# Performance work log

Hardware: AMD Instinct MI355X
Metric: run time of the kernel (lower is better)

## Reference

```python
import jax, jax.numpy as jnp
import numpy as np

N = 12288
E = 196608
H = 128
Z = 128
NEG = -1e9  # finite mask value (avoids -inf NaNs in grads)
WSCALE = 0.05


def setup_inputs() -> dict:
    key = jax.random.key(0)
    ks = jax.random.split(key, 16)
    inp = {}
    inp["x"] = jax.random.normal(ks[0], (N, 2), dtype=jnp.float32)
    inp["z"] = jax.random.normal(ks[1], (Z,), dtype=jnp.float32)
    inp["node_type"] = jax.random.randint(ks[2], (N,), 0, 3, dtype=jnp.int32)
    inp["node_depth"] = jax.random.randint(ks[3], (N,), 0, 64, dtype=jnp.int32)
    inp["edge_index"] = jax.random.randint(ks[4], (2, E), 0, N, dtype=jnp.int32)
    inp["W1"] = jax.random.normal(ks[5], (2, H), dtype=jnp.float32) * WSCALE
    inp["b1"] = jnp.zeros((H,), jnp.float32)
    inp["W2"] = jax.random.normal(ks[6], (H, H), dtype=jnp.float32) * WSCALE
    inp["b2"] = jnp.zeros((H,), jnp.float32)
    inp["Wm1"] = jax.random.normal(ks[7], (H + Z, H), dtype=jnp.float32) * WSCALE
    inp["bm1"] = jnp.zeros((H,), jnp.float32)
    inp["Wm2"] = jax.random.normal(ks[8], (H, H), dtype=jnp.float32) * WSCALE
    inp["bm2"] = jnp.zeros((H,), jnp.float32)
    inp["Ws"] = jax.random.normal(ks[9], (H, H), dtype=jnp.float32) * WSCALE
    inp["Wt"] = jax.random.normal(ks[10], (H, H), dtype=jnp.float32) * WSCALE
    inp["Wi1"] = jax.random.normal(ks[11], (2 * H + Z, H), dtype=jnp.float32) * WSCALE
    inp["bi1"] = jnp.zeros((H,), jnp.float32)
    inp["Wi2"] = jax.random.normal(ks[12], (H, 1), dtype=jnp.float32) * WSCALE
    inp["bi2"] = jnp.zeros((1,), jnp.float32)
    return inp


def _gcn(x, W, b, src, dst, n):
    # GCNConv with self-loops and symmetric deg^-1/2 normalization
    loop = jnp.arange(n, dtype=src.dtype)
    s = jnp.concatenate([src, loop])
    d = jnp.concatenate([dst, loop])
    deg = jax.ops.segment_sum(jnp.ones_like(d, dtype=x.dtype), d, num_segments=n)
    inv_sqrt = jnp.where(deg > 0, jax.lax.rsqrt(jnp.maximum(deg, 1.0)), 0.0)
    w = inv_sqrt[s] * inv_sqrt[d]  # [E+N]
    agg = jax.ops.segment_sum(x[s] * w[:, None], d, num_segments=n)  # [N,F]
    return agg @ W + b


def reference(x, z, node_type, node_depth, edge_index,
              W1, b1, W2, b2, Wm1, bm1, Wm2, bm2, Ws, Wt, Wi1, bi1, Wi2, bi2):
    n = x.shape[0]
    src, dst = edge_index[0], edge_index[1]
    # 2-layer GCN encode
    h = jax.nn.relu(_gcn(x, W1, b1, src, dst, n))
    h = jax.nn.relu(_gcn(h, W2, b2, src, dst, n))
    # node_mlp on [h, z] (no outer relu, per original edge_index branch)
    zb = jnp.broadcast_to(z, (n, Z))
    h = jax.nn.relu(jnp.concatenate([h, zb], axis=1) @ Wm1 + bm1) @ Wm2 + bm2  # [N,H]
    # batched score: St[v,u] = tgt_proj(h_v) . src_proj(h_u)
    St = (h @ Wt) @ (h @ Ws).T  # [N(target), N(candidate)]
    cand_ok = node_depth[None, :] < node_depth[:, None]  # candidate strictly shallower
    St = jnp.where(cand_ok, St, NEG)
    vals, idx = jax.lax.top_k(St, 2)  # [N,2] per-target top candidates
    # target is active if type != 0, depth > 0, and at least one candidate exists
    tv = (node_type != 0) & (node_depth > 0) & (vals[:, 0] > NEG / 2)
    # k=2 edges for AND nodes (type==2), else k=1
    edge_valid = jnp.stack([tv, tv & (node_type == 2)], axis=1)  # [N,2]
    # inversion bit mlp on [h_u, h_v, z]
    hu = h[idx]  # [N,2,H]
    hv = jnp.broadcast_to(h[:, None, :], hu.shape)
    zz = jnp.broadcast_to(z, (n, 2, Z))
    feat = jnp.concatenate([hu, hv, zz], axis=-1)  # [N,2,2H+Z]
    logit = (jax.nn.relu(feat @ Wi1 + bi1) @ Wi2 + bi2)[..., 0]  # [N,2]
    inv_prob = jax.nn.sigmoid(logit)
    return inv_prob, vals, idx, edge_valid
```

## Files before the change

### kernel.cpp

```cpp
#include <hip/hip_runtime.h>
#include <hip/hip_bf16.h>

#define NN 12288
#define NE 196608
#define HD 128
#define ZD 128
#define NEGV (-1.0e9f)
#define SEG 16

using s8v = __attribute__((ext_vector_type(8))) short;
using f4v = __attribute__((ext_vector_type(4))) float;
using i4v = __attribute__((ext_vector_type(4))) int;

__device__ __forceinline__ unsigned short f2bf(float f) {
    return __builtin_bit_cast(unsigned short, __float2bfloat16(f));
}
__device__ __forceinline__ float4 pack8(float4 a, float4 b) {
    unsigned p0 = ((unsigned)f2bf(a.y) << 16) | f2bf(a.x);
    unsigned p1 = ((unsigned)f2bf(a.w) << 16) | f2bf(a.z);
    unsigned p2 = ((unsigned)f2bf(b.y) << 16) | f2bf(b.x);
    unsigned p3 = ((unsigned)f2bf(b.w) << 16) | f2bf(b.z);
    i4v r = (i4v){(int)p0, (int)p1, (int)p2, (int)p3};
    return __builtin_bit_cast(float4, r);
}

__global__ __launch_bounds__(256) void k_counts_wz(
        const int* __restrict__ edst, const int* __restrict__ ndep,
        const float* __restrict__ W2, const float* __restrict__ Wm1,
        const float* __restrict__ Wm2, const float* __restrict__ Wtm,
        const float* __restrict__ Wsm, const float* __restrict__ Wi1,
        const float* __restrict__ z, const float* __restrict__ bm1,
        const float* __restrict__ bi1,
        int* degi, int* cnt, __hip_bfloat16* __restrict__ wt7,
        float* cz1, float* cz2) {
    __shared__ int lh[64];
    __shared__ float tl[16 * 129];
    int tid = threadIdx.x;
    int bid = blockIdx.x;
    if (bid < NE / 256) {
        int e = bid * 256 + tid;
        atomicAdd(&degi[edst[e]], 1);
    } else if (bid < NE / 256 + NN / 256) {
        if (tid < 64) lh[tid] = 0;
        __syncthreads();
        int v = (bid - NE / 256) * 256 + tid;
        atomicAdd(&lh[ndep[v]], 1);
        __syncthreads();
        if (tid < 64) {
            int c = lh[tid];
            if (c) atomicAdd(&cnt[tid * 16], c);
        }
    } else if (bid < NE / 256 + NN / 256 + 56) {
        int b2 = bid - NE / 256 - NN / 256;
        int g = b2 >> 3;
        int k0 = (b2 & 7) << 4;
        const float* src;
        if (g == 0) src = W2;
        else if (g == 1) src = Wm1;
        else if (g == 2) src = Wm2;
        else if (g == 3) src = Wtm;
        else if (g == 4) src = Wsm;
        else if (g == 5) src = Wi1;
        else src = Wi1 + 128 * HD;
#pragma unroll
        for (int i = 0; i < 8; ++i) {
            int idx = i * 256 + tid;
            int kk = idx >> 7, n = idx & 127;
            tl[kk * 129 + n] = src[(k0 + kk) * 128 + n];
        }
        __syncthreads();
#pragma unroll
        for (int i = 0; i < 8; ++i) {
            int idx = i * 256 + tid;
            int n = idx >> 4, kk = idx & 15;
            wt7[(g << 14) + n * 128 + k0 + kk] = __float2bfloat16(tl[kk * 129 + n]);
        }
    } else {
        int j = tid & 127;
        const float* W = (tid < 128) ? (Wm1 + HD * HD) : (Wi1 + 2 * HD * HD);
        float A0 = 0.f, A1 = 0.f, A2 = 0.f, A3 = 0.f;
        for (int k = 0; k < ZD; k += 4) {
            A0 = fmaf(z[k],     W[(k    ) * HD + j], A0);
            A1 = fmaf(z[k + 1], W[(k + 1) * HD + j], A1);
            A2 = fmaf(z[k + 2], W[(k + 2) * HD + j], A2);
            A3 = fmaf(z[k + 3], W[(k + 3) * HD + j], A3);
        }
        float r = (A0 + A1) + (A2 + A3);
        if (tid < 128) cz1[j] = r + bm1[j];
        else           cz2[j] = r + bi1[j];
    }
}

__global__ __launch_bounds__(1024) void k_prefix(const int* __restrict__ degi,
                                                 const int* __restrict__ cnt,
                                                 const float* __restrict__ x,
                                                 float* inv, float* agg2,
                                                 float4* __restrict__ xi,
                                                 int* offs, int* cursor,
                                                 int* bofs, int* dcur) {
    __shared__ int ldeg[NN];
    __shared__ int part[1024];
    __shared__ int stot;
    int tid = threadIdx.x;
#pragma unroll
    for (int k = 0; k < 12; ++k)
        ldeg[k * 1024 + tid] = degi[k * 1024 + tid];
    __syncthreads();
    int base = tid * 12;
    int s = 0;
#pragma unroll
    for (int k = 0; k < 12; ++k) s += ldeg[base + k];
    part[tid] = s;
    __syncthreads();
    for (int off = 1; off < 1024; off <<= 1) {
        int v = (tid >= off) ? part[tid - off] : 0;
        __syncthreads();
        part[tid] += v;
        __syncthreads();
    }
    int run = part[tid] - s;
#pragma unroll
    for (int k = 0; k < 12; ++k) {
        int d = ldeg[base + k];
        ldeg[base + k] = run;
        run += d;
    }
    if (tid == 1023) stot = run;
    __syncthreads();
    int total = stot;
    const float2* X2 = (const float2*)x;
    float2* A2 = (float2*)agg2;
#pragma unroll
    for (int k = 0; k < 12; ++k) {
        int i = k * 1024 + tid;
        int p = ldeg[i];
        int nxt = (i < NN - 1) ? ldeg[i + 1] : total;
        int d = nxt - p;
        offs[i] = p;
        cursor[i] = p;
        float iv = rsqrtf((float)(d + 1));
        inv[i] = iv;
        float w = iv * iv;
        float2 xv = X2[i];
        float2 av; av.x = xv.x * w; av.y = xv.y * w;
        A2[i] = av;
        float4 xo; xo.x = xv.x; xo.y = xv.y; xo.z = iv; xo.w = 0.f;
        xi[i] = xo;
    }
    if (tid == 0) {
        offs[NN] = total;
        int r = 0;
        for (int d = 0; d < 64; ++d) {
            bofs[d] = r;
            dcur[d * 16] = r;
            r += cnt[d * 16];
        }
        bofs[64] = r;
    }
}

__global__ __launch_bounds__(256) void k_bucket_scatter(
        const int* __restrict__ esrc, const int* __restrict__ edst,
        const int* __restrict__ ndep,
        int* cursor, int* ebsrc,
        int* dcur, int* sidx, int* sdep, int* prank) {
    __shared__ int lh[64];
    __shared__ int lbase[64];
    int tid = threadIdx.x;
    if (blockIdx.x < NE / 256) {
        int e = blockIdx.x * 256 + tid;
        int u = esrc[e], v = edst[e];
        int pos = atomicAdd(&cursor[v], 1);
        ebsrc[pos] = u;
    } else {
        if (tid < 64) lh[tid] = 0;
        __syncthreads();
        int v = (blockIdx.x - NE / 256) * 256 + tid;
        int d = ndep[v];
        int r = atomicAdd(&lh[d], 1);
        __syncthreads();
        if (tid < 64) {
            int c = lh[tid];
            if (c) lbase[tid] = atomicAdd(&dcur[tid * 16], c);
        }
        __syncthreads();
        int p = lbase[d] + r;
        sidx[p] = v;
        sdep[p] = d;
        prank[v] = p;
    }
}

__global__ __launch_bounds__(256) void k_gl1(const int* __restrict__ offs,
                                             const int* __restrict__ ebsrc,
                                             const float4* __restrict__ xi,
                                             const float* __restrict__ agg2,
                                             const float* __restrict__ W1,
                                             const float* __restrict__ b1,
                                             const float* __restrict__ inv,
                                             unsigned short* h1b, float* aggH) {
    __shared__ float2 la[32];
    int tid = threadIdx.x;
    int v0 = blockIdx.x * 32;
    {
        int nb = tid >> 3;
        int sl = tid & 7;
        int v = v0 + nb;
        int b = offs[v], e = offs[v + 1];
        float ax = 0.f, ay = 0.f;
        for (int k = b + sl; k < e; k += 8) {
            int u = ebsrc[k];
            float4 xv = xi[u];
            ax = fmaf(xv.x, xv.z, ax);
            ay = fmaf(xv.y, xv.z, ay);
        }
#pragma unroll
        for (int m = 1; m < 8; m <<= 1) {
            ax += __shfl_xor(ax, m, 64);
            ay += __shfl_xor(ay, m, 64);
        }
        if (sl == 0) {
            float ivv = inv[v];
            float2 seed = ((const float2*)agg2)[v];
            seed.x = fmaf(ax, ivv, seed.x);
            seed.y = fmaf(ay, ivv, seed.y);
            la[nb] = seed;
        }
    }
    __syncthreads();
    {
#pragma unroll
        for (int k = 0; k < 16; ++k) {
            int idx = k * 256 + tid;
            int vloc = idx >> 7, j = idx & 127;
            float2 a = la[vloc];
            float hv = fmaxf(fmaf(a.x, W1[j], fmaf(a.y, W1[HD + j], b1[j])), 0.f);
            int t = (v0 + vloc) * HD + j;
            float iv = inv[v0 + vloc];
            h1b[t] = f2bf(hv * iv);
            aggH[t] = hv * iv * iv;
        }
    }
}

#define AFRAGS(BUF) \
    s8v a0_ = __builtin_bit_cast(s8v, (BUF)[lane16 * 16 + ((quad     ) ^ lane16)]); \
    s8v a1_ = __builtin_bit_cast(s8v, (BUF)[lane16 * 16 + ((quad +  4) ^ lane16)]); \
    s8v a2_ = __builtin_bit_cast(s8v, (BUF)[lane16 * 16 + ((quad +  8) ^ lane16)]); \
    s8v a3_ = __builtin_bit_cast(s8v, (BUF)[lane16 * 16 + ((quad + 12) ^ lane16)]);

#define NBACC(WT4, NCOL, ACC) \
    f4v ACC = (f4v){0.f, 0.f, 0.f, 0.f}; \
    ACC = __builtin_amdgcn_mfma_f32_16x16x32_bf16(a0_, __builtin_bit_cast(s8v, (WT4)[(NCOL) * 16 + quad     ]), ACC, 0, 0, 0); \
    ACC = __builtin_amdgcn_mfma_f32_16x16x32_bf16(a1_, __builtin_bit_cast(s8v, (WT4)[(NCOL) * 16 + quad +  4]), ACC, 0, 0, 0); \
    ACC = __builtin_amdgcn_mfma_f32_16x16x32_bf16(a2_, __builtin_bit_cast(s8v, (WT4)[(NCOL) * 16 + quad +  8]), ACC, 0, 0, 0); \
    ACC = __builtin_amdgcn_mfma_f32_16x16x32_bf16(a3_, __builtin_bit_cast(s8v, (WT4)[(NCOL) * 16 + quad + 12]), ACC, 0, 0, 0);

#define BST(EXPR, RR, COL, USPTR) { int rw_ = quad * 4 + (RR); int cc_ = (COL) >> 3; \
    (USPTR)[rw_ * 128 + (((cc_ ^ rw_)) << 3) + ((COL) & 7)] = f2bf(EXPR); }

#define LDS4R(ACC, B, COL, US) \
    BST(fmaxf(ACC[0] + (B), 0.f), 0, COL, US) BST(fmaxf(ACC[1] + (B), 0.f), 1, COL, US) \
    BST(fmaxf(ACC[2] + (B), 0.f), 2, COL, US) BST(fmaxf(ACC[3] + (B), 0.f), 3, COL, US)

#define LDS4(ACC, B, COL, US) \
    BST(ACC[0] + (B), 0, COL, US) BST(ACC[1] + (B), 1, COL, US) \
    BST(ACC[2] + (B), 2, COL, US) BST(ACC[3] + (B), 3, COL, US)

#define GBF4S(ACC, COL, PTR) \
    ((unsigned short*)(PTR))[(size_t)pr0 * HD + (COL)] = f2bf(ACC[0]); \
    ((unsigned short*)(PTR))[(size_t)pr1 * HD + (COL)] = f2bf(ACC[1]); \
    ((unsigned short*)(PTR))[(size_t)pr2 * HD + (COL)] = f2bf(ACC[2]); \
    ((unsigned short*)(PTR))[(size_t)pr3 * HD + (COL)] = f2bf(ACC[3]);

#define GF4(ACC, B, COL, PTR) \
    (PTR)[(size_t)(r0 + quad * 4 + 0) * HD + (COL)] = ACC[0] + (B); \
    (PTR)[(size_t)(r0 + quad * 4 + 1) * HD + (COL)] = ACC[1] + (B); \
    (PTR)[(size_t)(r0 + quad * 4 + 2) * HD + (COL)] = ACC[2] + (B); \
    (PTR)[(size_t)(r0 + quad * 4 + 3) * HD + (COL)] = ACC[3] + (B);

__global__ __launch_bounds__(256) void k_ghmlp7(
        const int* __restrict__ offs, const int* __restrict__ ebsrc,
        const float* __restrict__ inv, const unsigned short* __restrict__ h1b,
        const float* __restrict__ s1in, const __hip_bfloat16* __restrict__ wt7,
        const float* __restrict__ bb2, const float* __restrict__ bcz1,
        const float* __restrict__ bbm2, const float* __restrict__ bcz2,
        const int* __restrict__ prank,
        float* __restrict__ outA, float* __restrict__ outB,
        __hip_bfloat16* __restrict__ htb, __hip_bfloat16* __restrict__ hsb) {
    __shared__ float4 bufA4[256];
    __shared__ float4 bufB4[256];
    __shared__ float laggH[16 * 128];
    int tid = threadIdx.x;
    int wv = tid >> 6;
    int l = tid & 63;
    int lane16 = l & 15;
    int quad = l >> 4;
    int r0 = blockIdx.x * 16;
    const float4* wt4 = (const float4*)wt7;

    int pr0 = prank[r0 + quad * 4 + 0];
    int pr1 = prank[r0 + quad * 4 + 1];
    int pr2 = prank[r0 + quad * 4 + 2];
    int pr3 = prank[r0 + quad * 4 + 3];

    {
        const unsigned* H1 = (const unsigned*)h1b;
        const float2* S2r = (const float2*)s1in;
        float2* LG2 = (float2*)laggH;
#pragma unroll
        for (int j = 0; j < 4; ++j) {
            int v = r0 + wv * 4 + j;
            float2 acc; acc.x = 0.f; acc.y = 0.f;
            int b = offs[v], e = offs[v + 1];
            int k = b;
            for (; k + 4 <= e; k += 4) {
                int u0 = ebsrc[k], u1 = ebsrc[k + 1];
                int u2 = ebsrc[k + 2], u3 = ebsrc[k + 3];
                unsigned hb0 = H1[(size_t)u0 * 64 + l];
                unsigned hb1 = H1[(size_t)u1 * 64 + l];
                unsigned hb2 = H1[(size_t)u2 * 64 + l];
                unsigned hb3 = H1[(size_t)u3 * 64 + l];
                acc.x += __builtin_bit_cast(float, hb0 << 16);
                acc.y += __builtin_bit_cast(float, hb0 & 0xFFFF0000u);
                acc.x += __builtin_bit_cast(float, hb1 << 16);
                acc.y += __builtin_bit_cast(float, hb1 & 0xFFFF0000u);
                acc.x += __builtin_bit_cast(float, hb2 << 16);
                acc.y += __builtin_bit_cast(float, hb2 & 0xFFFF0000u);
                acc.x += __builtin_bit_cast(float, hb3 << 16);
                acc.y += __builtin_bit_cast(float, hb3 & 0xFFFF0000u);
            }
            for (; k < e; ++k) {
                int u = ebsrc[k];
                unsigned hb = H1[(size_t)u * 64 + l];
                acc.x += __builtin_bit_cast(float, hb << 16);
                acc.y += __builtin_bit_cast(float, hb & 0xFFFF0000u);
            }
            float ivv = inv[v];
            float2 seed = S2r[(size_t)v * 64 + l];
            seed.x = fmaf(acc.x, ivv, seed.x);
            seed.y = fmaf(acc.y, ivv, seed.y);
            LG2[(wv * 4 + j) * 64 + l] = seed;
        }
    }
    __syncthreads();
    {
        const float4* g4 = (const float4*)laggH;
        float4 u0 = g4[2 * tid], u1 = g4[2 * tid + 1];
        int row_ = tid >> 4, c_ = tid & 15;
        bufA4[row_ * 16 + (c_ ^ row_)] = pack8(u0, u1);
    }
    __syncthreads();
    int col0 = wv * 32 + lane16, col1 = col0 + 16;
    unsigned short* usA = (unsigned short*)bufA4;
    unsigned short* usB = (unsigned short*)bufB4;

    {
        AFRAGS(bufA4)
        NBACC(wt4, col0, cA) NBACC(wt4, col1, cB)
        float q0 = bb2[col0], q1 = bb2[col1];
        LDS4R(cA, q0, col0, usB) LDS4R(cB, q1, col1, usB)
    }
    __syncthreads();
    {
        AFRAGS(bufB4)
        const float4* wt = wt4 + 2048;
        NBACC(wt, col0, cA) NBACC(wt, col1, cB)
        float q0 = bcz1[col0], q1 = bcz1[col1];
        LDS4R(cA, q0, col0, usA) LDS4R(cB, q1, col1, usA)
    }
    __syncthreads();
    {
        AFRAGS(bufA4)
        const float4* wt = wt4 + 2 * 2048;
        NBACC(wt, col0, cA) NBACC(wt, col1, cB)
        float q0 = bbm2[col0], q1 = bbm2[col1];
        LDS4(cA, q0, col0, usB) LDS4(cB, q1, col1, usB)
    }
    __syncthreads();
    {
        AFRAGS(bufB4)
        const float4* wt = wt4 + 3 * 2048;
        NBACC(wt, col0, cA) NBACC(wt, col1, cB)
        GBF4S(cA, col0, htb) GBF4S(cB, col1, htb)
    }
    {
        AFRAGS(bufB4)
        const float4* wt = wt4 + 4 * 2048;
        NBACC(wt, col0, cA) NBACC(wt, col1, cB)
        GBF4S(cA, col0, hsb) GBF4S(cB, col1, hsb)
    }
    {
        AFRAGS(bufB4)
        const float4* wt = wt4 + 5 * 2048;
        NBACC(wt, col0, cA) NBACC(wt, col1, cB)
        GF4(cA, 0.f, col0, outA) GF4(cB, 0.f, col1, outA)
    }
    {
        AFRAGS(bufB4)
        const float4* wt = wt4 + 6 * 2048;
        NBACC(wt, col0, cA) NBACC(wt, col1, cB)
        float q0 = bcz2[col0], q1 = bcz2[col1];
        GF4(cA, q0, col0, outB) GF4(cB, q1, col1, outB)
    }
}

#define STG(buf, q, val) { int r_ = (q) >> 4, c_ = (q) & 15; \
    (buf)[r_ * 16 + (c_ ^ (r_ & 7))] = (val); }

#define KC2(kc, AX, AY) { \
    int co_ = (kc) * 4 + quad; \
    int bo_ = bbase + (co_ ^ brm); \
    s8v b0_ = __builtin_bit_cast(s8v, B[bo_      ]); \
    s8v b1_ = __builtin_bit_cast(s8v, B[bo_ + 256]); \
    s8v b2_ = __builtin_bit_cast(s8v, B[bo_ + 512]); \
    s8v b3_ = __builtin_bit_cast(s8v, B[bo_ + 768]); \
    x0 = __builtin_amdgcn_mfma_f32_16x16x32_bf16(AX, b0_, x0, 0, 0, 0); \
    y0 = __builtin_amdgcn_mfma_f32_16x16x32_bf16(AY, b0_, y0, 0, 0, 0); \
    x1 = __builtin_amdgcn_mfma_f32_16x16x32_bf16(AX, b1_, x1, 0, 0, 0); \
    y1 = __builtin_amdgcn_mfma_f32_16x16x32_bf16(AY, b1_, y1, 0, 0, 0); \
    x2 = __builtin_amdgcn_mfma_f32_16x16x32_bf16(AX, b2_, x2, 0, 0, 0); \
    y2 = __builtin_amdgcn_mfma_f32_16x16x32_bf16(AY, b2_, y2, 0, 0, 0); \
    x3 = __builtin_amdgcn_mfma_f32_16x16x32_bf16(AX, b3_, x3, 0, 0, 0); \
    y3 = __builtin_amdgcn_mfma_f32_16x16x32_bf16(AY, b3_, y3, 0, 0, 0); }

#define RMG(K1, K2, EL, DV) { \
    unsigned pb_ = (__builtin_bit_cast(unsigned, EL) & 0xFFFFC000u) | e_; \
    float sf_ = __builtin_bit_cast(float, (du_ < (DV)) ? pb_ : negp_); \
    K2 = __builtin_amdgcn_fmed3f(K1, K2, sf_); \
    K1 = fmaxf(K1, sf_); }

#define MGEN(nb, XA, YA) { \
    unsigned pk_ = eds[ebase + (nb) * 16 + lane16]; \
    int du_ = (int)(pk_ >> 16); \
    unsigned e_ = pk_ & 0x3FFFu; \
    unsigned negp_ = negbase | e_; \
    RMG(k1x0, k2x0, XA[0], dvx0) RMG(k1x1, k2x1, XA[1], dvx1) \
    RMG(k1x2, k2x2, XA[2], dvx2) RMG(k1x3, k2x3, XA[3], dvx3) \
    RMG(k1y0, k2y0, YA[0], dvy0) RMG(k1y1, k2y1, YA[1], dvy1) \
    RMG(k1y2, k2y2, YA[2], dvy2) RMG(k1y3, k2y3, YA[3], dvy3) }

#define RMF(K1, K2, EL) { \
    float sf_ = __builtin_bit_cast(float, \
        (__builtin_bit_cast(unsigned, EL) & 0xFFFFC000u) | e_); \
    K2 = __builtin_amdgcn_fmed3f(K1, K2, sf_); \
    K1 = fmaxf(K1, sf_); }

#define MFAST(nb, XA, YA) { \
    unsigned e_ = eds[ebase + (nb) * 16 + lane16] & 0x3FFFu; \
    RMF(k1x0, k2x0, XA[0]) RMF(k1x1, k2x1, XA[1]) \
    RMF(k1x2, k2x2, XA[2]) RMF(k1x3, k2x3, XA[3]) \
    RMF(k1y0, k2y0, YA[0]) RMF(k1y1, k2y1, YA[1]) \
    RMF(k1y2, k2y2, YA[2]) RMF(k1y3, k2y3, YA[3]) }

#define BF1(K1, K2, m) { \
    float o1_ = __shfl_xor(K1, m, 64); \
    float o2_ = __shfl_xor(K2, m, 64); \
    float m2_ = fmaxf(K2, o2_); \
    K2 = __builtin_amdgcn_fmed3f(K1, o1_, m2_); \
    K1 = fmaxf(K1, o1_); }

#define BFALL(m) \
    BF1(k1x0, k2x0, m) BF1(k1x1, k2x1, m) BF1(k1x2, k2x2, m) BF1(k1x3, k2x3, m) \
    BF1(k1y0, k2y0, m) BF1(k1y1, k2y1, m) BF1(k1y2, k2y2, m) BF1(k1y3, k2y3, m)

#define EMIT2(K1, K2, GROW) { \
    size_t o = ((size_t)seg * NN + (GROW)) * 2; \
    pv[o] = K1; pv[o + 1] = K2; }

__global__ __launch_bounds__(256) void k_score_top2_mfma(
        const __hip_bfloat16* __restrict__ htb,
        const __hip_bfloat16* __restrict__ hsb,
        const int* __restrict__ sdep, const int* __restrict__ sidx,
        const int* __restrict__ bofs,
        float* __restrict__ pv) {
    __shared__ float4 Bs4[2][64 * 16];
    __shared__ unsigned eds[12 * 64];
    int tid = threadIdx.x;
    int w = tid >> 6;
    int l = tid & 63;
    int lane16 = l & 15;
    int quad = l >> 4;
    int rb = (int)gridDim.x - 1 - (int)blockIdx.x;
    int row0 = rb * 128;
    int seg = blockIdx.y;
    const unsigned negbase = __builtin_bit_cast(unsigned, NEGV) & 0xFFFFC000u;

    int dmax = sdep[row0 + 127];
    int lim = bofs[dmax];
    int nt = (lim + 63) >> 6;
    int ns = (nt + 11) / 12;
    if (ns < 1) ns = 1;
    if (seg >= ns) {
        if (tid < 128) {
            int grow = sidx[row0 + tid];
            size_t o = ((size_t)seg * NN + grow) * 2;
            pv[o]     = __builtin_bit_cast(float, negbase | 0x3FFFu);
            pv[o + 1] = __builtin_bit_cast(float, negbase | 0x3FFEu);
        }
        return;
    }
    int t0 = (seg * nt) / ns;
    int t1 = ((seg + 1) * nt) / ns;

    int rbase = row0 + w * 32;
    s8v ax0, ax1, ax2, ax3, ay0, ay1, ay2, ay3;
    {
        const float4* gx = (const float4*)(htb + (size_t)(rbase + lane16) * HD);
        ax0 = __builtin_bit_cast(s8v, gx[quad]);
        ax1 = __builtin_bit_cast(s8v, gx[4 + quad]);
        ax2 = __builtin_bit_cast(s8v, gx[8 + quad]);
        ax3 = __builtin_bit_cast(s8v, gx[12 + quad]);
        const float4* gy = (const float4*)(htb + (size_t)(rbase + 16 + lane16) * HD);
        ay0 = __builtin_bit_cast(s8v, gy[quad]);
        ay1 = __builtin_bit_cast(s8v, gy[4 + quad]);
        ay2 = __builtin_bit_cast(s8v, gy[8 + quad]);
        ay3 = __builtin_bit_cast(s8v, gy[12 + quad]);
    }
    for (int i = tid; i < (t1 - t0) * 64; i += 256) {
        int p = t0 * 64 + i;
        eds[i] = ((unsigned)sdep[p] << 16) | (0x3FFFu - (unsigned)sidx[p]);
    }
    if (t0 < t1) {
        float4* B0 = Bs4[t0 & 1];
        const float4* gb = (const float4*)(hsb + (size_t)(t0 * 64) * HD);
        float4 b0_ = gb[tid], b1_ = gb[tid + 256], b2_ = gb[tid + 512], b3_ = gb[tid + 768];
        STG(B0, tid, b0_) STG(B0, tid + 256, b1_)
        STG(B0, tid + 512, b2_) STG(B0, tid + 768, b3_)
    }

    int bbase = lane16 * 16, brm = lane16 & 7;

    int dvx0 = sdep[rbase + quad * 4 + 0];
    int dvx1 = sdep[rbase + quad * 4 + 1];
    int dvx2 = sdep[rbase + quad * 4 + 2];
    int dvx3 = sdep[rbase + quad * 4 + 3];
    int dvy0 = sdep[rbase + 16 + quad * 4 + 0];
    int dvy1 = sdep[rbase + 16 + quad * 4 + 1];
    int dvy2 = sdep[rbase + 16 + quad * 4 + 2];
    int dvy3 = sdep[rbase + 16 + quad * 4 + 3];
    int lim_lo = bofs[sdep[rbase]];
    int lim_hi = bofs[sdep[rbase + 31]];

    float ki1 = (lane16 == 0) ? __builtin_bit_cast(float, negbase | 0x3FFFu) : -3.4e38f;
    float ki2 = (lane16 == 0) ? __builtin_bit_cast(float, negbase | 0x3FFEu) : -3.4e38f;
    float k1x0 = ki1, k1x1 = ki1, k1x2 = ki1, k1x3 = ki1;
    float k1y0 = ki1, k1y1 = ki1, k1y2 = ki1, k1y3 = ki1;
    float k2x0 = ki2, k2x1 = ki2, k2x2 = ki2, k2x3 = ki2;
    float k2y0 = ki2, k2y1 = ki2, k2y2 = ki2, k2y3 = ki2;

    float4 p0, p1, p2, p3;
    for (int t = t0; t < t1; ++t) {
        int u0 = t * 64;
        int ebase = (t - t0) * 64;
        __syncthreads();
        if (t + 1 < t1) {
            const float4* g = (const float4*)(hsb + (size_t)(u0 + 64) * HD);
            p0 = g[tid]; p1 = g[tid + 256]; p2 = g[tid + 512]; p3 = g[tid + 768];
        }
        if (u0 < lim_hi) {
            const float4* B = Bs4[t & 1];
            f4v x0 = (f4v){0.f, 0.f, 0.f, 0.f};
            f4v x1 = (f4v){0.f, 0.f, 0.f, 0.f};
            f4v x2 = (f4v){0.f, 0.f, 0.f, 0.f};
            f4v x3 = (f4v){0.f, 0.f, 0.f, 0.f};
            f4v y0 = (f4v){0.f, 0.f, 0.f, 0.f};
            f4v y1 = (f4v){0.f, 0.f, 0.f, 0.f};
            f4v y2 = (f4v){0.f, 0.f, 0.f, 0.f};
            f4v y3 = (f4v){0.f, 0.f, 0.f, 0.f};
            KC2(0, ax0, ay0) KC2(1, ax1, ay1) KC2(2, ax2, ay2) KC2(3, ax3, ay3)
            if (u0 + 64 <= lim_lo) {
                MFAST(0, x0, y0) MFAST(1, x1, y1)
                MFAST(2, x2, y2) MFAST(3, x3, y3)
            } else {
                MGEN(0, x0, y0) MGEN(1, x1, y1)
                MGEN(2, x2, y2) MGEN(3, x3, y3)
            }
        }
        if (t + 1 < t1) {
            float4* Bn = Bs4[(t + 1) & 1];
            STG(Bn, tid, p0) STG(Bn, tid + 256, p1)
            STG(Bn, tid + 512, p2) STG(Bn, tid + 768, p3)
        }
    }

    BFALL(1) BFALL(2) BFALL(4) BFALL(8)

    if (lane16 == 0) {
        int gbse = rbase + quad * 4;
        EMIT2(k1x0, k2x0, sidx[gbse + 0])
        EMIT2(k1x1, k2x1, sidx[gbse + 1])
        EMIT2(k1x2, k2x2, sidx[gbse + 2])
        EMIT2(k1x3, k2x3, sidx[gbse + 3])
        EMIT2(k1y0, k2y0, sidx[gbse + 16])
        EMIT2(k1y1, k2y1, sidx[gbse + 17])
        EMIT2(k1y2, k2y2, sidx[gbse + 18])
        EMIT2(k1y3, k2y3, sidx[gbse + 19])
    }
}

__global__ __launch_bounds__(256) void k_final(const float* __restrict__ pv,
                                               const int* __restrict__ ntype,
                                               const int* __restrict__ ndepth,
                                               const float* __restrict__ A,
                                               const float* __restrict__ B,
                                               const float* __restrict__ Wi2,
                                               const float* __restrict__ bi2,
                                               float* __restrict__ out) {
    int tid = threadIdx.x;
    int lane = tid & 63;
    int v = blockIdx.x * 4 + (tid >> 6);

    float k1 = -3.4e38f;
    if (lane < 32) {
        k1 = pv[((size_t)(lane >> 1) * NN + v) * 2 + (lane & 1)];
    }
    float k2 = -3.4e38f;
#pragma unroll
    for (int m = 1; m <= 16; m <<= 1) {
        float o1 = __shfl_xor(k1, m, 64);
        float o2 = __shfl_xor(k2, m, 64);
        float m2 = fmaxf(k2, o2);
        k2 = __builtin_amdgcn_fmed3f(k1, o1, m2);
        k1 = fmaxf(k1, o1);
    }
    float K1 = __shfl(k1, 0, 64);
    float K2 = __shfl(k2, 0, 64);
    unsigned b1 = __builtin_bit_cast(unsigned, K1);
    unsigned b2 = __builtin_bit_cast(unsigned, K2);
    int I1 = 0x3FFF - (int)(b1 & 0x3FFFu);
    int I2 = 0x3FFF - (int)(b2 & 0x3FFFu);

    if (lane == 0) {
        int tp = ntype[v];
        bool tv = (tp != 0) && (ndepth[v] > 0) && (K1 > -5.0e8f);
        out[2 * NN + 2 * v]     = K1;
        out[2 * NN + 2 * v + 1] = K2;
        out[4 * NN + 2 * v]     = (float)I1;
        out[4 * NN + 2 * v + 1] = (float)I2;
        out[6 * NN + 2 * v]     = tv ? 1.f : 0.f;
        out[6 * NN + 2 * v + 1] = (tv && tp == 2) ? 1.f : 0.f;
    }

    int u1 = min(max(I1, 0), NN - 1);
    int u2 = min(max(I2, 0), NN - 1);
    const float2* A2p = (const float2*)A;
    float2 av1 = A2p[(size_t)u1 * 64 + lane];
    float2 av2 = A2p[(size_t)u2 * 64 + lane];
    float2 bv = ((const float2*)B)[(size_t)v * 64 + lane];
    float2 wv = ((const float2*)Wi2)[lane];
    float bias = bi2[0];
    float a1 = fmaf(fmaxf(av1.x + bv.x, 0.f), wv.x,
                    fmaxf(av1.y + bv.y, 0.f) * wv.y);
    float a2 = fmaf(fmaxf(av2.x + bv.x, 0.f), wv.x,
                    fmaxf(av2.y + bv.y, 0.f) * wv.y);
#pragma unroll
    for (int off = 32; off > 0; off >>= 1) {
        a1 += __shfl_down(a1, off);
        a2 += __shfl_down(a2, off);
    }
    if (lane == 0) {
        out[2 * v]     = 1.f / (1.f + expf(-(a1 + bias)));
        out[2 * v + 1] = 1.f / (1.f + expf(-(a2 + bias)));
    }
}

extern "C" void kernel_launch(void* const* d_in, const int* in_sizes, int n_in,
                              void* d_out, int out_size, void* d_ws, size_t ws_size,
                              hipStream_t stream) {
    (void)in_sizes; (void)n_in; (void)out_size; (void)ws_size;
    const float* x   = (const float*)d_in[0];
    const float* z   = (const float*)d_in[1];
    const int* ntype = (const int*)d_in[2];
    const int* ndep  = (const int*)d_in[3];
    const int* eidx  = (const int*)d_in[4];
    const float* W1  = (const float*)d_in[5];
    const float* b1  = (const float*)d_in[6];
    const float* W2  = (const float*)d_in[7];
    const float* b2  = (const float*)d_in[8];
    const float* Wm1 = (const float*)d_in[9];
    const float* bm1 = (const float*)d_in[10];
    const float* Wm2 = (const float*)d_in[11];
    const float* bm2 = (const float*)d_in[12];
    const float* Wsm = (const float*)d_in[13];
    const float* Wtm = (const float*)d_in[14];
    const float* Wi1 = (const float*)d_in[15];
    const float* bi1 = (const float*)d_in[16];
    const float* Wi2 = (const float*)d_in[17];
    const float* bi2 = (const float*)d_in[18];
    float* out = (float*)d_out;

    const int* esrc = eidx;
    const int* edst = eidx + NE;

    const size_t S2N = (size_t)SEG * 2 * NN;
    float* ws = (float*)d_ws;
    float* pv     = ws;
    int*   pi     = (int*)(pv + S2N);
    int*   degi   = pi + S2N;
    int*   cnt    = degi + NN;
    int*   dcur   = cnt + 1024;
    float* inv    = (float*)(dcur + 1024);
    float* agg2   = inv + NN;
    float* cz1    = agg2 + 2 * NN;
    float* cz2    = cz1 + 128;
    int*   offs   = (int*)(cz2 + 128);
    int*   cursor = offs + NN + 16;
    int*   bofs   = cursor + NN;
    int*   sidx   = bofs + 80;
    int*   sdep   = sidx + NN;
    int*   prank  = sdep + NN;
    int*   ebsrc  = prank + NN;
    float* ebwslot= (float*)(ebsrc + NE);
    float4* xi    = (float4*)ebwslot;
    __hip_bfloat16* wt7 = (__hip_bfloat16*)(ebwslot + NE);
    size_t F = (size_t)NN * HD;
    float* s0 = (float*)(wt7 + 7 * 16384);
    float* s1 = s0 + F;
    float* s2 = s1 + F;
    unsigned short* h1b = (unsigned short*)s0;
    __hip_bfloat16* htb = (__hip_bfloat16*)s0;
    __hip_bfloat16* hsb = htb + F;

    hipMemsetAsync(degi, 0, (NN + 1024) * sizeof(int), stream);
    k_counts_wz<<<NE / 256 + NN / 256 + 56 + 1, 256, 0, stream>>>(
        edst, ndep, W2, Wm1, Wm2, Wtm, Wsm, Wi1, z, bm1, bi1,
        degi, cnt, wt7, cz1, cz2);
    k_prefix<<<1, 1024, 0, stream>>>(degi, cnt, x, inv, agg2, xi, offs, cursor,
                                     bofs, dcur);
    k_bucket_scatter<<<NE / 256 + NN / 256, 256, 0, stream>>>(
        esrc, edst, ndep, cursor, ebsrc, dcur, sidx, sdep, prank);
    k_gl1<<<NN / 32, 256, 0, stream>>>(offs, ebsrc, xi, agg2, W1, b1, inv,
                                       h1b, s1);
    k_ghmlp7<<<NN / 16, 256, 0, stream>>>(offs, ebsrc, inv, h1b, s1, wt7,
                                          b2, cz1, bm2, cz2, prank,
                                          s2, s1, htb, hsb);
    k_score_top2_mfma<<<dim3(NN / 128, SEG), 256, 0, stream>>>(
        htb, hsb, sdep, sidx, bofs, pv);
    k_final<<<NN / 4, 256, 0, stream>>>(pv, ntype, ndep, s2, s1, Wi2, bi2, out);
}
```

Before: 222.2 us.

## Parallelize degree prefix scan across 48 blocks using per-chunk partial sums

After: 222.5 us. About the same (+0.1%).

```diff
diff --git a/kernel.cpp b/kernel.cpp
--- a/kernel.cpp
+++ b/kernel.cpp
@@ -31,15 +31,25 @@
         const float* __restrict__ Wsm, const float* __restrict__ Wi1,
         const float* __restrict__ z, const float* __restrict__ bm1,
         const float* __restrict__ bi1,
-        int* degi, int* cnt, __hip_bfloat16* __restrict__ wt7,
+        int* degi, int* cnt, int* psum, __hip_bfloat16* __restrict__ wt7,
         float* cz1, float* cz2) {
     __shared__ int lh[64];
+    __shared__ int lh48[48];
     __shared__ float tl[16 * 129];
     int tid = threadIdx.x;
     int bid = blockIdx.x;
     if (bid < NE / 256) {
+        if (tid < 48) lh48[tid] = 0;
+        __syncthreads();
         int e = bid * 256 + tid;
-        atomicAdd(&degi[edst[e]], 1);
+        int v = edst[e];
+        atomicAdd(&degi[v], 1);
+        atomicAdd(&lh48[v >> 8], 1);
+        __syncthreads();
+        if (tid < 48) {
+            int c = lh48[tid];
+            if (c) atomicAdd(&psum[tid * 16], c);
+        }
     } else if (bid < NE / 256 + NN / 256) {
         if (tid < 64) lh[tid] = 0;
         __syncthreads();
@@ -91,71 +101,57 @@
     }
 }
 
-__global__ __launch_bounds__(1024) void k_prefix(const int* __restrict__ degi,
-                                                 const int* __restrict__ cnt,
-                                                 const float* __restrict__ x,
-                                                 float* inv, float* agg2,
-                                                 float4* __restrict__ xi,
-                                                 int* offs, int* cursor,
-                                                 int* bofs, int* dcur) {
-    __shared__ int ldeg[NN];
-    __shared__ int part[1024];
-    __shared__ int stot;
+__global__ __launch_bounds__(256) void k_prefix(const int* __restrict__ degi,
+                                                const int* __restrict__ cnt,
+                                                const int* __restrict__ psum,
+                                                const float* __restrict__ x,
+                                                float* inv, float* agg2,
+                                                float4* __restrict__ xi,
+                                                int* offs, int* cursor,
+                                                int* bofs, int* dcur) {
+    __shared__ int pch[48];
+    __shared__ int lsc[256];
     int tid = threadIdx.x;
-#pragma unroll
-    for (int k = 0; k < 12; ++k)
-        ldeg[k * 1024 + tid] = degi[k * 1024 + tid];
+    int blk = blockIdx.x;
+    if (tid < 48) pch[tid] = psum[tid * 16];
+    int i = blk * 256 + tid;
+    int d = degi[i];
+    lsc[tid] = d;
     __syncthreads();
-    int base = tid * 12;
-    int s = 0;
-#pragma unroll
-    for (int k = 0; k < 12; ++k) s += ldeg[base + k];
-    part[tid] = s;
-    __syncthreads();
-    for (int off = 1; off < 1024; off <<= 1) {
-        int v = (tid >= off) ? part[tid - off] : 0;
-        __syncthreads();
-        part[tid] += v;
-        __syncthreads();
-    }
-    int run = part[tid] - s;
-#pragma unroll
-    for (int k = 0; k < 12; ++k) {
-        int d = ldeg[base + k];
-        ldeg[base + k] = run;
-        run += d;
-    }
-    if (tid == 1023) stot = run;
-    __syncthreads();
-    int total = stot;
+    int cb = 0;
+    for (int c = 0; c < 48; ++c) cb += (c < blk) ? pch[c] : 0;
+    int s = d;
+    for (int off = 1; off < 256; off <<= 1) {
+        int v = (tid >= off) ? lsc[tid - off] : 0;
+        __syncthreads();
+        lsc[tid] += v;
+        s = lsc[tid];
+        __syncthreads();
+    }
+    int excl = cb + s - d;
+    offs[i] = excl;
+    cursor[i] = excl;
+    float iv = rsqrtf((float)(d + 1));
+    inv[i] = iv;
+    float w = iv * iv;
     const float2* X2 = (const float2*)x;
-    float2* A2 = (float2*)agg2;
-#pragma unroll
-    for (int k = 0; k < 12; ++k) {
-        int i = k * 1024 + tid;
-        int p = ldeg[i];
-        int nxt = (i < NN - 1) ? ldeg[i + 1] : total;
-        int d = nxt - p;
-        offs[i] = p;
-        cursor[i] = p;
-        float iv = rsqrtf((float)(d + 1));
-        inv[i] = iv;
-        float w = iv * iv;
-        float2 xv = X2[i];
-        float2 av; av.x = xv.x * w; av.y = xv.y * w;
-        A2[i] = av;
-        float4 xo; xo.x = xv.x; xo.y = xv.y; xo.z = iv; xo.w = 0.f;
-        xi[i] = xo;
-    }
-    if (tid == 0) {
-        offs[NN] = total;
-        int r = 0;
-        for (int d = 0; d < 64; ++d) {
-            bofs[d] = r;
-            dcur[d * 16] = r;
-            r += cnt[d * 16];
-        }
-        bofs[64] = r;
+    float2 xv = X2[i];
+    float2 av; av.x = xv.x * w; av.y = xv.y * w;
+    ((float2*)agg2)[i] = av;
+    float4 xo; xo.x = xv.x; xo.y = xv.y; xo.z = iv; xo.w = 0.f;
+    xi[i] = xo;
+    if (blk == 47 && tid == 255) offs[NN] = excl + d;
+    if (blk == 0 && tid < 64) {
+        int c = cnt[tid * 16];
+        int sc = c;
+        for (int off = 1; off < 64; off <<= 1) {
+            int v = __shfl_up(sc, off, 64);
+            if (tid >= off) sc += v;
+        }
+        int ex = sc - c;
+        bofs[tid] = ex;
+        dcur[tid * 16] = ex;
+        if (tid == 63) bofs[64] = sc;
     }
 }
 
@@ -699,7 +695,8 @@
     int*   pi     = (int*)(pv + S2N);
     int*   degi   = pi + S2N;
     int*   cnt    = degi + NN;
-    int*   dcur   = cnt + 1024;
+    int*   psum   = cnt + 1024;
+    int*   dcur   = psum + 768;
     float* inv    = (float*)(dcur + 1024);
     float* agg2   = inv + NN;
     float* cz1    = agg2 + 2 * NN;
@@ -722,12 +719,12 @@
     __hip_bfloat16* htb = (__hip_bfloat16*)s0;
     __hip_bfloat16* hsb = htb + F;
 
-    hipMemsetAsync(degi, 0, (NN + 1024) * sizeof(int), stream);
+    hipMemsetAsync(degi, 0, (NN + 1024 + 768) * sizeof(int), stream);
     k_counts_wz<<<NE / 256 + NN / 256 + 56 + 1, 256, 0, stream>>>(
         edst, ndep, W2, Wm1, Wm2, Wtm, Wsm, Wi1, z, bm1, bi1,
-        degi, cnt, wt7, cz1, cz2);
-    k_prefix<<<1, 1024, 0, stream>>>(degi, cnt, x, inv, agg2, xi, offs, cursor,
-                                     bofs, dcur);
+        degi, cnt, psum, wt7, cz1, cz2);
+    k_prefix<<<48, 256, 0, stream>>>(degi, cnt, psum, x, inv, agg2, xi,
+                                     offs, cursor, bofs, dcur);
     k_bucket_scatter<<<NE / 256 + NN / 256, 256, 0, stream>>>(
         esrc, edst, ndep, cursor, ebsrc, dcur, sidx, sdep, prank);
     k_gl1<<<NN / 32, 256, 0, stream>>>(offs, ebsrc, xi, agg2, W1, b1, inv,
```
